# Kernel tuning notes

Measured on AMD Instinct MI355X. Metric: run time of the kernel, lower is better.

Reference implementation:

```python
import jax, jax.numpy as jnp
import numpy as np

B, H, W, DIM = 1, 256, 256, 192
HEADS = 6
K, DIL = 7, 2            # NAttention kernel / dilation
WS, DF = 8, 2            # stripe window size, anchor down factor
AWS = WS // DF           # anchor window size (4)
N1, N2 = WS * WS, AWS * AWS
L = H * W
CPB_HID = 512


def _nbr(size, k, d):
    # 1D neighborhood-attention neighbor indices with dilation (edge-clamped)
    i = np.arange(size); g = i % d; p = i // d
    gsize = size // d  # d divides size
    start = np.clip(p - k // 2, 0, gsize - k)
    nbr_p = start[:, None] + np.arange(k)[None, :]
    nbr = g[:, None] + d * nbr_p                    # absolute key index
    rb = nbr_p - p[:, None] + (k - 1)               # rpb index in [0, 2k-2]
    return nbr.astype(np.int32), rb.astype(np.int32)

NBR_H, RB_H = _nbr(H, K, DIL)
NBR_W, RB_W = _nbr(W, K, DIL)


def _na_attention(q, k, v, rpb):
    # q,k,v: (B, heads, H, W, hd); rpb: (heads, 2K-1, 2K-1)
    bias = rpb[:, RB_H, :]                          # (heads,H,K,2K-1)
    bias = jnp.take(bias, RB_W, axis=3)             # (heads,H,K,W,K)
    bias = jnp.transpose(bias, (0, 1, 3, 2, 4))     # (heads,H,W,K,K)
    logits = []
    for ki in range(K):
        kh = jnp.take(k, NBR_H[:, ki], axis=2)
        for kj in range(K):
            khw = jnp.take(kh, NBR_W[:, kj], axis=3)
            logits.append(jnp.einsum('bnhwc,bnhwc->bnhw', q, khw))
    a = jnp.stack(logits, axis=-1).reshape(*q.shape[:4], K, K) + bias[None]
    a = jax.nn.softmax(a.reshape(*q.shape[:4], K * K), axis=-1).reshape(*q.shape[:4], K, K)
    out = jnp.zeros_like(q)
    for ki in range(K):
        vh = jnp.take(v, NBR_H[:, ki], axis=2)
        for kj in range(K):
            vhw = jnp.take(vh, NBR_W[:, kj], axis=3)
            out = out + a[..., ki, kj, None] * vhw
    return out

na_attention = jax.checkpoint(_na_attention)


def window_partition(x, ws):
    b, h, w, c = x.shape
    x = x.reshape(b, h // ws, ws, w // ws, ws, c)
    return jnp.transpose(x, (0, 1, 3, 2, 4, 5)).reshape(-1, ws * ws, c)


def window_reverse(x, ws, h, w):
    c = x.shape[-1]
    b = x.shape[0] // ((h // ws) * (w // ws))
    x = x.reshape(b, h // ws, w // ws, ws, ws, c)
    return jnp.transpose(x, (0, 1, 3, 2, 4, 5)).reshape(b, h, w, c)


def _l2n(x):
    n = jnp.linalg.norm(x, axis=-1, keepdims=True)
    return x / jnp.maximum(n, 1e-12)


def _affine(attn, table, index, ls, w1, b1, w2):
    # attn: (Bw, heads, Na, Nb)
    attn = attn * jnp.exp(jnp.minimum(ls, float(np.log(100.0))))[None]
    bt = jax.nn.relu(table.reshape(-1, 2) @ w1 + b1) @ w2           # (T, heads)
    bias = bt[index.reshape(-1)].reshape(index.shape[0], index.shape[1], HEADS)
    bias = 16.0 * jax.nn.sigmoid(jnp.transpose(bias, (2, 0, 1)))    # (heads,Na,Nb)
    return attn + bias[None]


def _cos_attn(q, k, v, table, index, ls, w1, b1, w2):
    attn = jnp.einsum('bhnc,bhmc->bhnm', _l2n(q), _l2n(k))
    attn = jax.nn.softmax(_affine(attn, table, index, ls, w1, b1, w2), axis=-1)
    return attn @ v


def _forward(x, h_size, w_size, table, index_a2w, index_w2a, qkv_w, qkv_b,
             anchor_dw_w, anchor_dw_b, anchor_pw_w, anchor_pw_b,
             na_qkv_w, na_qkv_b, na_after_w, na_after_b, na_rpb,
             ls1, cpb1_w1, cpb1_b1, cpb1_w2, ls2, cpb2_w1, cpb2_b1, cpb2_w2,
             proj_w, proj_b):
    Bx, Lx, C = x.shape
    Hs, Ws_ = int(h_size), int(w_size)
    qkv = x @ qkv_w + qkv_b                     # (B,L,3C)
    half = C * 3 // 2
    qkv_window, qkv_stripe = qkv[..., :half], qkv[..., half:]
    # anchor projection: depthwise conv (k=DF+1, stride=DF) + pointwise
    xi = x.reshape(Bx, Hs, Ws_, C)
    a = jax.lax.conv_general_dilated(
        xi, anchor_dw_w, (DF, DF), ((1, 1), (1, 1)),
        dimension_numbers=('NHWC', 'HWIO', 'NHWC'), feature_group_count=C) + anchor_dw_b
    a = a @ anchor_pw_w + anchor_pw_b           # (B, H/DF, W/DF, C//2)
    # ---- neighborhood attention branch ----
    hd = C // HEADS
    xw = qkv_window.reshape(Bx, Hs, Ws_, half)
    q2 = (xw @ na_qkv_w + na_qkv_b).reshape(Bx, Hs, Ws_, 3, HEADS, hd)
    q2 = jnp.transpose(q2, (3, 0, 4, 1, 2, 5))  # (3,B,heads,H,W,hd)
    qn, kn, vn = q2[0] * hd ** -0.5, q2[1], q2[2]
    xna = na_attention(qn, kn, vn, na_rpb)
    xna = jnp.transpose(xna, (0, 2, 3, 1, 4)).reshape(Bx, Hs, Ws_, C)
    xna = (xna @ na_after_w + na_after_b).reshape(Bx, Lx, C // 2)
    # ---- anchor stripe attention branch ----
    qs = window_partition(qkv_stripe.reshape(Bx, Hs, Ws_, half), WS)  # (Bw,N1,1.5C)
    an = window_partition(a, AWS)                                     # (Bw,N2,C//2)
    Bw = qs.shape[0]
    hs = C // 2 // HEADS
    q3 = jnp.transpose(qs.reshape(Bw, N1, 3, HEADS, hs), (2, 0, 3, 1, 4))
    q_s, k_s, v_s = q3[0], q3[1], q3[2]
    an = jnp.transpose(an.reshape(Bw, N2, HEADS, hs), (0, 2, 1, 3))
    x1 = _cos_attn(an, k_s, v_s, table, index_a2w, ls1, cpb1_w1, cpb1_b1, cpb1_w2)
    x2 = _cos_attn(q_s, an, x1, table, index_w2a, ls2, cpb2_w1, cpb2_b1, cpb2_w2)
    x2 = jnp.transpose(x2, (0, 2, 1, 3)).reshape(Bw, N1, C // 2)
    xs = window_reverse(x2, WS, Hs, Ws_).reshape(Bx, Lx, C // 2)
    return jnp.concatenate([xna, xs], axis=-1) @ proj_w + proj_b


def setup_inputs() -> dict:
    key = jax.random.key(0)
    ks = jax.random.split(key, 16)
    f = lambda i, shp, s=0.02: jax.random.normal(ks[i], shp, dtype=jnp.float32) * s
    x = jax.random.normal(ks[0], (B, L, DIM), dtype=jnp.float32)
    # swin-v2 style normalized log-spaced relative coords table
    rc = np.arange(-(WS - 1), WS, dtype=np.float32) / (WS - 1)
    t = np.stack(np.meshgrid(rc, rc, indexing='ij'), axis=-1)[None]
    table = jnp.asarray(np.sign(t) * np.log2(1 + np.abs(t) * 8) / 3.0, dtype=jnp.float32)
    wc = np.arange(WS); ac = np.arange(AWS) * DF
    cw = np.stack(np.meshgrid(wc, wc, indexing='ij'), -1).reshape(-1, 2)
    ca = np.stack(np.meshgrid(ac, ac, indexing='ij'), -1).reshape(-1, 2)
    def _idx(c1, c2):
        d = c1[:, None, :] - c2[None, :, :]
        return jnp.asarray((d[..., 0] + WS - 1) * (2 * WS - 1) + (d[..., 1] + WS - 1), dtype=jnp.int32)
    return {
        'x': x, 'h_size': H, 'w_size': W, 'table': table,
        'index_a2w': _idx(ca, cw), 'index_w2a': _idx(cw, ca),
        'qkv_w': f(1, (DIM, 3 * DIM)), 'qkv_b': jnp.zeros((3 * DIM,), jnp.float32),
        'anchor_dw_w': f(2, (DF + 1, DF + 1, 1, DIM), 0.1),
        'anchor_dw_b': jnp.zeros((DIM,), jnp.float32),
        'anchor_pw_w': f(3, (DIM, DIM // 2)), 'anchor_pw_b': jnp.zeros((DIM // 2,), jnp.float32),
        'na_qkv_w': f(4, (3 * DIM // 2, 3 * DIM)), 'na_qkv_b': jnp.zeros((3 * DIM,), jnp.float32),
        'na_after_w': f(5, (DIM, DIM // 2)), 'na_after_b': jnp.zeros((DIM // 2,), jnp.float32),
        'na_rpb': f(6, (HEADS, 2 * K - 1, 2 * K - 1)),
        'ls1': jnp.log(10.0) * jnp.ones((HEADS, 1, 1), jnp.float32),
        'cpb1_w1': f(7, (2, CPB_HID), 0.1), 'cpb1_b1': jnp.zeros((CPB_HID,), jnp.float32),
        'cpb1_w2': f(8, (CPB_HID, HEADS), 0.1),
        'ls2': jnp.log(10.0) * jnp.ones((HEADS, 1, 1), jnp.float32),
        'cpb2_w1': f(9, (2, CPB_HID), 0.1), 'cpb2_b1': jnp.zeros((CPB_HID,), jnp.float32),
        'cpb2_w2': f(10, (CPB_HID, HEADS), 0.1),
        'proj_w': f(11, (DIM, DIM)), 'proj_b': jnp.zeros((DIM,), jnp.float32),
    }


def reference(x, h_size, w_size, table, index_a2w, index_w2a, qkv_w, qkv_b,
              anchor_dw_w, anchor_dw_b, anchor_pw_w, anchor_pw_b,
              na_qkv_w, na_qkv_b, na_after_w, na_after_b, na_rpb,
              ls1, cpb1_w1, cpb1_b1, cpb1_w2, ls2, cpb2_w1, cpb2_b1, cpb2_w2,
              proj_w, proj_b):
    return _forward(x, h_size, w_size, table, index_a2w, index_w2a, qkv_w, qkv_b,
                    anchor_dw_w, anchor_dw_b, anchor_pw_w, anchor_pw_b,
                    na_qkv_w, na_qkv_b, na_after_w, na_after_b, na_rpb,
                    ls1, cpb1_w1, cpb1_b1, cpb1_w2, ls2, cpb2_w1, cpb2_b1, cpb2_w2,
                    proj_w, proj_b)
```

## Files before the change

kernel.cpp:

```cpp
#include <hip/hip_runtime.h>
#include <math.h>


typedef unsigned short bf16_t;
typedef __attribute__((ext_vector_type(8))) short short8;
typedef __attribute__((ext_vector_type(4))) float f32x4;

__device__ inline float bf2f(bf16_t v) { return __uint_as_float((unsigned)v << 16); }
__device__ inline bf16_t f2bf(float f) {
    unsigned u = __float_as_uint(f);
    unsigned r = (u + 0x7fffu + ((u >> 16) & 1u)) >> 16;
    return (bf16_t)r;
}
__device__ inline float cvt(float v) { return v; }
__device__ inline float cvt(bf16_t v) { return bf2f(v); }
__device__ inline void sto(float* p, float v) { *p = v; }
__device__ inline void sto(bf16_t* p, float v) { *p = f2bf(v); }

__device__ inline void ld_bf8(const bf16_t* p, float* d) {
    uint4 r = *(const uint4*)p;
    d[0] = __uint_as_float(r.x << 16); d[1] = __uint_as_float(r.x & 0xffff0000u);
    d[2] = __uint_as_float(r.y << 16); d[3] = __uint_as_float(r.y & 0xffff0000u);
    d[4] = __uint_as_float(r.z << 16); d[5] = __uint_as_float(r.z & 0xffff0000u);
    d[6] = __uint_as_float(r.w << 16); d[7] = __uint_as_float(r.w & 0xffff0000u);
}
__device__ inline unsigned pk2(float a, float b) {
    return (unsigned)f2bf(a) | ((unsigned)f2bf(b) << 16);
}

template <int KD, int NA, typename TO>
__global__ __launch_bounds__(256) void mfma_gemm_k(
    const bf16_t* __restrict__ A, const bf16_t* __restrict__ Bt,
    const float* __restrict__ bias, TO* __restrict__ C,
    int lda, int ldb, int ldc)
{
    const int t = threadIdx.x;
    const int lane = t & 63, wave = t >> 6;
    const int wr = wave >> 1, wc = wave & 1;
    const int m0 = blockIdx.y * 128 + wr * 64;
    const int n0 = blockIdx.x * 96 + wc * 48;
    const int lm = lane & 15;
    const int q  = lane >> 4;

    f32x4 acc[4][3] = {};
    const bf16_t* ap = A + (size_t)(m0 + lm) * lda + q * 8;
    const bf16_t* bp = Bt + (size_t)(n0 + lm) * ldb + q * 8;

#pragma unroll
    for (int k0 = 0; k0 < KD; k0 += 32) {
        short8 af[4], bf[3];
#pragma unroll
        for (int mi = 0; mi < 4; mi++)
            af[mi] = *(const short8*)(ap + (size_t)(mi * 16) * lda + k0);
#pragma unroll
        for (int ni = 0; ni < 3; ni++)
            bf[ni] = *(const short8*)(bp + (size_t)(ni * 16) * ldb + k0);
#pragma unroll
        for (int mi = 0; mi < 4; mi++)
#pragma unroll
            for (int ni = 0; ni < 3; ni++)
                acc[mi][ni] = __builtin_amdgcn_mfma_f32_16x16x32_bf16(
                    af[mi], bf[ni], acc[mi][ni], 0, 0, 0);
    }

#pragma unroll
    for (int mi = 0; mi < 4; mi++) {
#pragma unroll
        for (int ni = 0; ni < 3; ni++) {
            int col = n0 + ni * 16 + lm;
            float bv = bias[col];
            if (NA) {
                int which = col / 192;
                int hh = (col % 192) / 32;
                int d  = col % 32;
                size_t pbase = ((size_t)which * 6 + hh) * ((size_t)65536 * 32) + d;
#pragma unroll
                for (int r = 0; r < 4; r++) {
                    int row = m0 + mi * 16 + q * 4 + r;
                    int ii = row >> 8, jj = row & 255;
                    int par = ((ii & 1) << 1) | (jj & 1);
                    int pix = par * 16384 + (ii >> 1) * 128 + (jj >> 1);
                    sto(&C[pbase + (size_t)pix * 32], acc[mi][ni][r] + bv);
                }
            } else {
#pragma unroll
                for (int r = 0; r < 4; r++) {
                    int row = m0 + mi * 16 + q * 4 + r;
                    sto(&C[(size_t)row * ldc + col], acc[mi][ni][r] + bv);
                }
            }
        }
    }
}

__global__ __launch_bounds__(256) void cvt_bf16_k(
    const float* __restrict__ src, bf16_t* __restrict__ dst, int n8)
{
    int tid = blockIdx.x * 256 + threadIdx.x;
    if (tid >= n8) return;
    float4 a = ((const float4*)src)[tid * 2];
    float4 b = ((const float4*)src)[tid * 2 + 1];
    uint4 o;
    o.x = pk2(a.x, a.y); o.y = pk2(a.z, a.w);
    o.z = pk2(b.x, b.y); o.w = pk2(b.z, b.w);
    ((uint4*)dst)[tid] = o;
}

__global__ __launch_bounds__(256) void tcvt_k(
    const float* __restrict__ W, bf16_t* __restrict__ Wt,
    int Kd, int N, int ld, int coloff)
{
    int tid = blockIdx.x * 256 + threadIdx.x;
    if (tid >= Kd * N) return;
    int k = tid % Kd, n = tid / Kd;
    Wt[tid] = f2bf(W[(size_t)k * ld + coloff + n]);
}

__global__ __launch_bounds__(256) void tpose_qkvw_k(
    const float* __restrict__ W, float* __restrict__ WT)
{
    int tid = blockIdx.x * 256 + threadIdx.x;
    if (tid >= 288 * 192) return;
    int k = tid % 192, j = tid / 192;
    WT[tid] = W[(size_t)k * 576 + j];
}

__global__ __launch_bounds__(256) void fold_wna_t_k(
    const float* __restrict__ qkv_wT, const float* __restrict__ na_qkv_w,
    bf16_t* __restrict__ Wna_t)
{
    int tid = blockIdx.x * 256 + threadIdx.x;
    if (tid >= 576 * 192) return;
    int k = tid % 192, n = tid / 192;
    float acc = 0.f;
    for (int j = 0; j < 288; j++)
        acc += qkv_wT[j * 192 + k] * na_qkv_w[j * 576 + n];
    Wna_t[tid] = f2bf(acc);
}

__global__ __launch_bounds__(256) void fold_bna_k(
    const float* __restrict__ qkv_b, const float* __restrict__ na_qkv_w,
    const float* __restrict__ na_qkv_b, float* __restrict__ bna)
{
    int j = blockIdx.x * 256 + threadIdx.x;
    if (j >= 576) return;
    float acc = na_qkv_b[j];
    for (int k = 0; k < 288; k++)
        acc += qkv_b[k] * na_qkv_w[k * 576 + j];
    bna[j] = acc;
}

__global__ __launch_bounds__(256) void cpb_k(
    const float* __restrict__ table, const float* __restrict__ w1,
    const float* __restrict__ b1, const float* __restrict__ w2,
    float* __restrict__ bt)
{
    int tid = blockIdx.x * 256 + threadIdx.x;
    if (tid >= 225 * 6) return;
    int h = tid % 6, t = tid / 6;
    float t0 = table[t * 2], t1 = table[t * 2 + 1];
    float acc = 0.f;
    for (int m = 0; m < 512; m++) {
        float hv = t0 * w1[m] + t1 * w1[512 + m] + b1[m];
        hv = fmaxf(hv, 0.f);
        acc += hv * w2[m * 6 + h];
    }
    bt[tid] = acc;
}

__global__ __launch_bounds__(256) void sigb_k(
    const float* __restrict__ bt, const int* __restrict__ idx,
    float* __restrict__ bp)
{
    int tid = blockIdx.x * 256 + threadIdx.x;
    if (tid >= 6144) return;
    int h = tid >> 10, p = tid & 1023;
    bp[tid] = 16.0f / (1.0f + __expf(-bt[idx[p] * 6 + h]));
}

#define BM 64
#define BN 64
#define BKK 16
template <typename TA, typename TO>
__global__ __launch_bounds__(256) void gemm_k(
    const TA* __restrict__ A, const float* __restrict__ B,
    const float* __restrict__ bias, TO* __restrict__ C,
    int M, int N, int Kd, int lda, int ldb, int ldc)
{
    __shared__ float As[BKK][BM + 1];
    __shared__ float Bs[BKK][BN + 1];
    const int t  = threadIdx.x;
    const int tx = t & 15, ty = t >> 4;
    const int m0 = blockIdx.y * BM, n0 = blockIdx.x * BN;
    float acc[4][4] = {};

    for (int k0 = 0; k0 < Kd; k0 += BKK) {
#pragma unroll
        for (int i = 0; i < 4; i++) {
            int m = (t >> 4) + i * 16;
            int k = t & 15;
            int gm = m0 + m, gk = k0 + k;
            As[k][m] = (gm < M && gk < Kd) ? cvt(A[(size_t)gm * lda + gk]) : 0.f;
        }
#pragma unroll
        for (int i = 0; i < 4; i++) {
            int k = (t >> 6) + i * 4;
            int n = t & 63;
            int gk = k0 + k, gn = n0 + n;
            Bs[k][n] = (gk < Kd && gn < N) ? B[(size_t)gk * ldb + gn] : 0.f;
        }
        __syncthreads();
#pragma unroll
        for (int k = 0; k < BKK; k++) {
            float a[4], b[4];
#pragma unroll
            for (int i = 0; i < 4; i++) a[i] = As[k][ty * 4 + i];
#pragma unroll
            for (int j = 0; j < 4; j++) b[j] = Bs[k][tx * 4 + j];
#pragma unroll
            for (int i = 0; i < 4; i++)
#pragma unroll
                for (int j = 0; j < 4; j++) acc[i][j] += a[i] * b[j];
        }
        __syncthreads();
    }
#pragma unroll
    for (int i = 0; i < 4; i++) {
        int gm = m0 + ty * 4 + i;
        if (gm >= M) continue;
#pragma unroll
        for (int j = 0; j < 4; j++) {
            int gn = n0 + tx * 4 + j;
            if (gn >= N) continue;
            sto(&C[(size_t)gm * ldc + gn], acc[i][j] + bias[gn]);
        }
    }
}

__global__ __launch_bounds__(256) void dwconv_k(
    const float* __restrict__ x, const float* __restrict__ w,
    const float* __restrict__ b, float* __restrict__ adw)
{
    int tid = blockIdx.x * 256 + threadIdx.x;
    if (tid >= 16384 * 48) return;
    int c4 = tid % 48;
    int p = tid / 48;
    int ow = p & 127, oh = p >> 7;
    int c = c4 * 4;
    float4 s = *(const float4*)(b + c);
#pragma unroll
    for (int kh = 0; kh < 3; kh++) {
        int ih = oh * 2 - 1 + kh;
        if (ih < 0 || ih >= 256) continue;
#pragma unroll
        for (int kw = 0; kw < 3; kw++) {
            int iw = ow * 2 - 1 + kw;
            if (iw < 0 || iw >= 256) continue;
            float4 xv = *(const float4*)(x + (size_t)(ih * 256 + iw) * 192 + c);
            float4 wv = *(const float4*)(w + (kh * 3 + kw) * 192 + c);
            s.x += xv.x * wv.x; s.y += xv.y * wv.y;
            s.z += xv.z * wv.z; s.w += xv.w * wv.w;
        }
    }
    *(float4*)(adw + (size_t)p * 192 + c) = s;
}

__global__ __launch_bounds__(256) void na_attn_k(
    const bf16_t* __restrict__ nap, const float* __restrict__ rpb,
    bf16_t* __restrict__ outp)
{
    __shared__ float rpb_s[176];
    __shared__ __align__(16) unsigned P_s[4][16][20];

    const int t = threadIdx.x;
    const int wv = t >> 6, lane = t & 63;
    const int lm = lane & 15, lq = lane >> 4;
    const int z = blockIdx.z;
    const int h = z >> 2, par = z & 3;

    if (t < 169) rpb_s[t] = rpb[h * 169 + t];
    __syncthreads();

    const int pi  = blockIdx.y;
    const int pj0 = blockIdx.x * 64 + wv * 16;
    const int si  = min(max(pi - 3, 0), 121);
    const int rbh0 = si - pi + 6;
    const int c0  = min(max(pj0 - 3, 0), 121) & ~7;

    const size_t plane = (size_t)65536 * 32;
    const size_t poff  = (size_t)(par * 16384) * 32;
    const bf16_t* qpl = nap + (size_t)h * plane + poff;
    const bf16_t* kpl = nap + (size_t)(6 + h) * plane + poff;
    const bf16_t* vpl = nap + (size_t)(12 + h) * plane + poff;

    const short8 qf = *(const short8*)(qpl + ((size_t)(pi * 128 + pj0 + lm)) * 32 + lq * 8);

    int offc[4][2]; bool vm[4][2];
#pragma unroll
    for (int r = 0; r < 4; r++) {
        int q = lq * 4 + r, pj = pj0 + q;
        int sj = min(max(pj - 3, 0), 121);
#pragma unroll
        for (int t2 = 0; t2 < 2; t2++) {
            int c = c0 + 2 * lm + t2;
            vm[r][t2] = (c >= sj) && (c <= sj + 6);
            offc[r][t2] = min(max(c - pj + 6, 0), 12);
        }
    }
    const int kc0 = min(c0 + 2 * lm,     127) * 64;
    const int kc1 = min(c0 + 2 * lm + 1, 127) * 64;
    int vcoff[8];
#pragma unroll
    for (int i = 0; i < 8; i++) vcoff[i] = min(c0 + lq * 8 + i, 127) * 64;

    const float scale = 0.17677669529663687f;
    f32x4 o0 = {}, o1 = {};
    float sums[4] = {0.f, 0.f, 0.f, 0.f};
    const f32x4 zz = {};

#pragma unroll 2
    for (int rr = 0; rr < 7; rr++) {
        const size_t rb2 = (size_t)((si + rr) * 128) * 64;
        const char* krow = (const char*)kpl + rb2;
        const char* vrow = (const char*)vpl + rb2;

        short8 kf0 = *(const short8*)(krow + kc0 + lq * 16);
        short8 kf1 = *(const short8*)(krow + kc1 + lq * 16);
        f32x4 s0 = __builtin_amdgcn_mfma_f32_16x16x32_bf16(qf, kf0, zz, 0, 0, 0);
        f32x4 s1 = __builtin_amdgcn_mfma_f32_16x16x32_bf16(qf, kf1, zz, 0, 0, 0);

        const float* br = rpb_s + (rbh0 + rr) * 13;
        float e0[4], e1[4];
#pragma unroll
        for (int r = 0; r < 4; r++) {
            float a0 = __expf(fmaf(s0[r], scale, br[offc[r][0]]));
            float a1 = __expf(fmaf(s1[r], scale, br[offc[r][1]]));
            a0 = vm[r][0] ? a0 : 0.f;
            a1 = vm[r][1] ? a1 : 0.f;
            e0[r] = a0; e1[r] = a1;
            sums[r] += a0 + a1;
        }
#pragma unroll
        for (int r = 0; r < 4; r++) {
            unsigned pr;
            asm("v_cvt_pk_bf16_f32 %0, %1, %2" : "=v"(pr) : "v"(e0[r]), "v"(e1[r]));
            P_s[wv][lq * 4 + r][lm] = pr;
        }
        const short8 pf = *(const short8*)((const bf16_t*)P_s[wv][lm] + lq * 8);

        short8 vf0, vf1;
        const char* v0b = vrow + lm * 2;
        const char* v1b = vrow + 32 + lm * 2;
#pragma unroll
        for (int i = 0; i < 8; i++) {
            ((bf16_t*)&vf0)[i] = *(const bf16_t*)(v0b + vcoff[i]);
            ((bf16_t*)&vf1)[i] = *(const bf16_t*)(v1b + vcoff[i]);
        }
        o0 = __builtin_amdgcn_mfma_f32_16x16x32_bf16(pf, vf0, o0, 0, 0, 0);
        o1 = __builtin_amdgcn_mfma_f32_16x16x32_bf16(pf, vf1, o1, 0, 0, 0);
    }

#pragma unroll
    for (int r = 0; r < 4; r++) {
        float s = sums[r];
        s += __shfl_xor(s, 1, 64);
        s += __shfl_xor(s, 2, 64);
        s += __shfl_xor(s, 4, 64);
        s += __shfl_xor(s, 8, 64);
        sums[r] = 1.0f / s;
    }

    const int gi = par >> 1, gj = par & 1;
    const int i0 = pi * 2 + gi;
    bf16_t* ob = outp + ((size_t)i0 * 256 + gj) * 192 + h * 32 + lm;
#pragma unroll
    for (int r = 0; r < 4; r++) {
        int q = lq * 4 + r;
        size_t px = (size_t)(pj0 + q) * 2 * 192;
        ob[px]      = f2bf(o0[r] * sums[r]);
        ob[px + 16] = f2bf(o1[r] * sums[r]);
    }
}

__global__ __launch_bounds__(256) void attn1_k(
    const float* __restrict__ apw,
    const bf16_t* __restrict__ qkvs,
    const float* __restrict__ b1p,
    const float* __restrict__ ls1,
    float* __restrict__ x1)
{
    int tid = blockIdx.x * 256 + threadIdx.x;
    int s  = tid & 7;
    int n2 = (tid >> 3) & 15;
    int h  = (tid >> 7) % 6;
    int w  = tid / 768;
    int wi = w >> 5, wj = w & 31;
    float scale = __expf(fminf(ls1[h], 4.605170185988091f));

    int ay = wi * 4 + (n2 >> 2), ax = wj * 4 + (n2 & 3);
    const float* ap = apw + (size_t)(ay * 128 + ax) * 96 + h * 16;
    float qv[16]; float nrm = 0.f;
#pragma unroll
    for (int d = 0; d < 16; d += 4) {
        float4 v = *(const float4*)(ap + d);
        qv[d] = v.x; qv[d + 1] = v.y; qv[d + 2] = v.z; qv[d + 3] = v.w;
        nrm += v.x * v.x + v.y * v.y + v.z * v.z + v.w * v.w;
    }
    float innorm = 1.0f / fmaxf(sqrtf(nrm), 1e-12f);
#pragma unroll
    for (int d = 0; d < 16; d++) qv[d] *= innorm;

    const float* bp = b1p + h * 1024 + n2 * 64 + s * 8;
    int ky = wi * 8 + s;
    const bf16_t* kbase = qkvs + (size_t)(ky * 256 + wj * 8) * 288 + 96 + h * 16;

    float sum = 0.f;
    float acc[16] = {};
#pragma unroll
    for (int j = 0; j < 8; j++) {
        const bf16_t* kp = kbase + j * 288;
        float kv[16];
        ld_bf8(kp, kv); ld_bf8(kp + 8, kv + 8);
        float dot = 0.f, kn = 0.f;
#pragma unroll
        for (int d = 0; d < 16; d++) { dot += qv[d] * kv[d]; kn += kv[d] * kv[d]; }
        dot *= 1.0f / fmaxf(sqrtf(kn), 1e-12f);
        float e = __expf(fmaf(dot, scale, bp[j]));
        sum += e;
        const bf16_t* vp = kp + 96;
        float vv[16];
        ld_bf8(vp, vv); ld_bf8(vp + 8, vv + 8);
#pragma unroll
        for (int d = 0; d < 16; d++) acc[d] += e * vv[d];
    }
#pragma unroll
    for (int msk = 1; msk < 8; msk <<= 1) {
        sum += __shfl_xor(sum, msk, 64);
#pragma unroll
        for (int d = 0; d < 16; d++) acc[d] += __shfl_xor(acc[d], msk, 64);
    }
    if (s == 0) {
        float inv = 1.0f / sum;
        float* xp = x1 + ((size_t)w * 6 + h) * 256 + n2 * 16;
#pragma unroll
        for (int d = 0; d < 16; d += 4)
            *(float4*)(xp + d) = make_float4(acc[d] * inv, acc[d + 1] * inv,
                                             acc[d + 2] * inv, acc[d + 3] * inv);
    }
}

__global__ __launch_bounds__(256) void attn2_k(
    const float* __restrict__ apw,
    const bf16_t* __restrict__ qkvs,
    const float* __restrict__ b2p,
    const float* __restrict__ ls2,
    const float* __restrict__ x1,
    bf16_t* __restrict__ cat)
{
    int tid = blockIdx.x * 256 + threadIdx.x;
    if (tid >= 1024 * 6 * 64) return;
    int n1 = tid & 63;
    int h = (tid >> 6) % 6;
    int w = tid / 384;
    int wi = w >> 5, wj = w & 31;
    float scale = __expf(fminf(ls2[h], 4.605170185988091f));

    int qy = wi * 8 + (n1 >> 3), qx = wj * 8 + (n1 & 7);
    const bf16_t* qp = qkvs + (size_t)(qy * 256 + qx) * 288 + h * 16;
    float qv[16];
    ld_bf8(qp, qv); ld_bf8(qp + 8, qv + 8);
    float nrm = 0.f;
#pragma unroll
    for (int d = 0; d < 16; d++) nrm += qv[d] * qv[d];
    float innorm = 1.0f / fmaxf(sqrtf(nrm), 1e-12f);
#pragma unroll
    for (int d = 0; d < 16; d++) qv[d] *= innorm;

    const float* bp = b2p + h * 1024 + n1 * 16;
    float sum = 0.f;
    float acc[16] = {};
#pragma unroll
    for (int m = 0; m < 16; m++) {
        int ay = wi * 4 + (m >> 2), ax = wj * 4 + (m & 3);
        const float* ap = apw + (size_t)(ay * 128 + ax) * 96 + h * 16;
        float dot = 0.f, kn = 0.f;
#pragma unroll
        for (int d = 0; d < 16; d += 4) {
            float4 v = *(const float4*)(ap + d);
            dot += qv[d] * v.x + qv[d + 1] * v.y + qv[d + 2] * v.z + qv[d + 3] * v.w;
            kn += v.x * v.x + v.y * v.y + v.z * v.z + v.w * v.w;
        }
        dot *= 1.0f / fmaxf(sqrtf(kn), 1e-12f);
        float e = __expf(fmaf(dot, scale, bp[m]));
        sum += e;
        const float* vp = x1 + ((size_t)w * 6 + h) * 256 + m * 16;
#pragma unroll
        for (int d = 0; d < 16; d += 4) {
            float4 v = *(const float4*)(vp + d);
            acc[d] += e * v.x; acc[d + 1] += e * v.y;
            acc[d + 2] += e * v.z; acc[d + 3] += e * v.w;
        }
    }
    float inv = 1.0f / sum;
#pragma unroll
    for (int d = 0; d < 16; d++) acc[d] *= inv;
    bf16_t* op = cat + (size_t)(qy * 256 + qx) * 192 + 96 + h * 16;
    uint4 o0, o1;
    o0.x = pk2(acc[0], acc[1]);   o0.y = pk2(acc[2], acc[3]);
    o0.z = pk2(acc[4], acc[5]);   o0.w = pk2(acc[6], acc[7]);
    o1.x = pk2(acc[8], acc[9]);   o1.y = pk2(acc[10], acc[11]);
    o1.z = pk2(acc[12], acc[13]); o1.w = pk2(acc[14], acc[15]);
    *(uint4*)(op) = o0;
    *(uint4*)(op + 8) = o1;
}

extern "C" void kernel_launch(void* const* d_in, const int* in_sizes, int n_in,
                              void* d_out, int out_size, void* d_ws, size_t ws_size,
                              hipStream_t stream) {
    const float* x          = (const float*)d_in[0];
    const float* table      = (const float*)d_in[3];
    const int*   idx_a2w    = (const int*)d_in[4];
    const int*   idx_w2a    = (const int*)d_in[5];
    const float* qkv_w      = (const float*)d_in[6];
    const float* qkv_b      = (const float*)d_in[7];
    const float* adw_w      = (const float*)d_in[8];
    const float* adw_b      = (const float*)d_in[9];
    const float* apw_w      = (const float*)d_in[10];
    const float* apw_b      = (const float*)d_in[11];
    const float* na_qkv_w   = (const float*)d_in[12];
    const float* na_qkv_b   = (const float*)d_in[13];
    const float* na_after_w = (const float*)d_in[14];
    const float* na_after_b = (const float*)d_in[15];
    const float* na_rpb     = (const float*)d_in[16];
    const float* ls1        = (const float*)d_in[17];
    const float* cpb1_w1    = (const float*)d_in[18];
    const float* cpb1_b1    = (const float*)d_in[19];
    const float* cpb1_w2    = (const float*)d_in[20];
    const float* ls2        = (const float*)d_in[21];
    const float* cpb2_w1    = (const float*)d_in[22];
    const float* cpb2_b1    = (const float*)d_in[23];
    const float* cpb2_w2    = (const float*)d_in[24];
    const float* proj_w     = (const float*)d_in[25];
    const float* proj_b     = (const float*)d_in[26];
    float* out = (float*)d_out;
    (void)in_sizes; (void)n_in; (void)out_size; (void)ws_size;

    char* base = (char*)d_ws;
    size_t off = 0;
    auto alloc = [&](size_t bytes) {
        off = (off + 255) & ~(size_t)255;
        void* p = base + off; off += bytes; return p;
    };
    float*  bna    = (float*)alloc(576 * 4);
    float*  bt1    = (float*)alloc(225 * 6 * 4);
    float*  bt2    = (float*)alloc(225 * 6 * 4);
    float*  b1p    = (float*)alloc(6144 * 4);
    float*  b2p    = (float*)alloc(6144 * 4);
    float*  qkv_wT = (float*)alloc(288 * 192 * 4);
    bf16_t* Wna_t  = (bf16_t*)alloc(576 * 192 * 2);
    bf16_t* Ws_t   = (bf16_t*)alloc(288 * 192 * 2);
    bf16_t* Waft_t = (bf16_t*)alloc(96 * 192 * 2);
    bf16_t* Wproj_t= (bf16_t*)alloc(192 * 192 * 2);
    bf16_t* qkvs   = (bf16_t*)alloc((size_t)65536 * 288 * 2);
    char*   naR    = (char*)alloc((size_t)65536 * 576 * 2);
    char*   R      = (char*)alloc((size_t)65536 * 192 * 2);
    float*  apw    = (float*)alloc((size_t)16384 * 96 * 4);
    bf16_t* naqkv   = (bf16_t*)naR;
    float*  x1      = (float*)naR;
    bf16_t* cat     = (bf16_t*)(naR + (8 << 20));
    bf16_t* xb      = (bf16_t*)R;
    float*  adw     = (float*)R;
    bf16_t* xna_pre = (bf16_t*)R;

    tpose_qkvw_k<<<216, 256, 0, stream>>>(qkv_w, qkv_wT);
    fold_wna_t_k<<<432, 256, 0, stream>>>(qkv_wT, na_qkv_w, Wna_t);
    fold_bna_k<<<3, 256, 0, stream>>>(qkv_b, na_qkv_w, na_qkv_b, bna);
    cpb_k<<<6, 256, 0, stream>>>(table, cpb1_w1, cpb1_b1, cpb1_w2, bt1);
    cpb_k<<<6, 256, 0, stream>>>(table, cpb2_w1, cpb2_b1, cpb2_w2, bt2);
    sigb_k<<<24, 256, 0, stream>>>(bt1, idx_a2w, b1p);
    sigb_k<<<24, 256, 0, stream>>>(bt2, idx_w2a, b2p);
    tcvt_k<<<216, 256, 0, stream>>>(qkv_w, Ws_t, 192, 288, 576, 288);
    tcvt_k<<<72, 256, 0, stream>>>(na_after_w, Waft_t, 192, 96, 96, 0);
    tcvt_k<<<144, 256, 0, stream>>>(proj_w, Wproj_t, 192, 192, 192, 0);
    cvt_bf16_k<<<6144, 256, 0, stream>>>(x, xb, 65536 * 192 / 8);

    mfma_gemm_k<192, 0, bf16_t><<<dim3(3, 512), 256, 0, stream>>>(
        xb, Ws_t, qkv_b + 288, qkvs, 192, 192, 288);

    mfma_gemm_k<192, 1, bf16_t><<<dim3(6, 512), 256, 0, stream>>>(
        xb, Wna_t, bna, naqkv, 192, 192, 576);

    dwconv_k<<<3072, 256, 0, stream>>>(x, adw_w, adw_b, adw);
    gemm_k<float, float><<<dim3(2, 256), 256, 0, stream>>>(
        adw, apw_w, apw_b, apw, 16384, 96, 192, 192, 96, 96);

    na_attn_k<<<dim3(2, 128, 24), 256, 0, stream>>>(naqkv, na_rpb, xna_pre);

    mfma_gemm_k<192, 0, bf16_t><<<dim3(1, 512), 256, 0, stream>>>(
        xna_pre, Waft_t, na_after_b, cat, 192, 192, 192);

    attn1_k<<<3072, 256, 0, stream>>>(apw, qkvs, b1p, ls1, x1);
    attn2_k<<<1536, 256, 0, stream>>>(apw, qkvs, b2p, ls2, x1, cat);

    mfma_gemm_k<192, 0, float><<<dim3(2, 512), 256, 0, stream>>>(
        cat, Wproj_t, proj_b, out, 192, 192, 192);
}
```

Measured before the change: 666.5 us.

## Rewrite anchor-to-window attention with bf16 MFMA and transposed bias table

Replaces the scalar per-thread attn1 kernel with a wave-per-window kernel that computes QK logits and the PV product using 16x16x32 bf16 MFMA instructions. Probabilities are staged through shared memory and the bias is preloaded into LDS. A new bias kernel writes a transposed bias layout to match the MFMA output layout. This cuts scalar FMA and shuffle reductions, but rounds normalized q/k and the probabilities to bf16, which lowers precision.

```diff
diff --git a/kernel.cpp b/kernel.cpp
--- a/kernel.cpp
+++ b/kernel.cpp
@@ -178,6 +178,17 @@
     bp[tid] = 16.0f / (1.0f + __expf(-bt[idx[p] * 6 + h]));
 }
 
+__global__ __launch_bounds__(256) void sigb1T_k(
+    const float* __restrict__ bt, const int* __restrict__ idx,
+    float* __restrict__ bp)
+{
+    int tid = blockIdx.x * 256 + threadIdx.x;
+    if (tid >= 6144) return;
+    int h = tid >> 10, p = tid & 1023;
+    int m = p >> 4, n2 = p & 15;
+    bp[tid] = 16.0f / (1.0f + __expf(-bt[idx[n2 * 64 + m] * 6 + h]));
+}
+
 #define BM 64
 #define BN 64
 #define BKK 16
@@ -385,67 +396,113 @@
 __global__ __launch_bounds__(256) void attn1_k(
     const float* __restrict__ apw,
     const bf16_t* __restrict__ qkvs,
-    const float* __restrict__ b1p,
+    const float* __restrict__ b1pT,
     const float* __restrict__ ls1,
     float* __restrict__ x1)
 {
-    int tid = blockIdx.x * 256 + threadIdx.x;
-    int s  = tid & 7;
-    int n2 = (tid >> 3) & 15;
-    int h  = (tid >> 7) % 6;
-    int w  = tid / 768;
-    int wi = w >> 5, wj = w & 31;
-    float scale = __expf(fminf(ls1[h], 4.605170185988091f));
-
-    int ay = wi * 4 + (n2 >> 2), ax = wj * 4 + (n2 & 3);
-    const float* ap = apw + (size_t)(ay * 128 + ax) * 96 + h * 16;
-    float qv[16]; float nrm = 0.f;
-#pragma unroll
-    for (int d = 0; d < 16; d += 4) {
-        float4 v = *(const float4*)(ap + d);
-        qv[d] = v.x; qv[d + 1] = v.y; qv[d + 2] = v.z; qv[d + 3] = v.w;
-        nrm += v.x * v.x + v.y * v.y + v.z * v.z + v.w * v.w;
-    }
-    float innorm = 1.0f / fmaxf(sqrtf(nrm), 1e-12f);
-#pragma unroll
-    for (int d = 0; d < 16; d++) qv[d] *= innorm;
-
-    const float* bp = b1p + h * 1024 + n2 * 64 + s * 8;
-    int ky = wi * 8 + s;
-    const bf16_t* kbase = qkvs + (size_t)(ky * 256 + wj * 8) * 288 + 96 + h * 16;
-
+    __shared__ float bT_s[1024];
+    __shared__ __align__(16) unsigned P_s[4][16][36];
+
+    const int t = threadIdx.x;
+    const int wv = t >> 6, lane = t & 63;
+    const int lm = lane & 15, lq = lane >> 4;
+    const int h = blockIdx.y;
+    const int w = blockIdx.x * 4 + wv;
+    const int wi = w >> 5, wj = w & 31;
+
+#pragma unroll
+    for (int i = 0; i < 4; i++) bT_s[i * 256 + t] = b1pT[h * 1024 + i * 256 + t];
+    __syncthreads();
+
+    const float scale = __expf(fminf(ls1[h], 4.605170185988091f));
+
+    short8 af = {};
+    float an2 = 0.f;
+    {
+        int ay = wi * 4 + (lm >> 2), ax = wj * 4 + (lm & 3);
+        const float* ap = apw + (size_t)(ay * 128 + ax) * 96 + h * 16;
+        if (lq < 2) {
+            float4 v0 = *(const float4*)(ap + lq * 8);
+            float4 v1 = *(const float4*)(ap + lq * 8 + 4);
+            float vs[8] = {v0.x, v0.y, v0.z, v0.w, v1.x, v1.y, v1.z, v1.w};
+            unsigned* au = (unsigned*)&af;
+#pragma unroll
+            for (int j2 = 0; j2 < 4; j2++) {
+                unsigned u = pk2(vs[2 * j2], vs[2 * j2 + 1]);
+                au[j2] = u;
+                float lo = __uint_as_float(u << 16);
+                float hi = __uint_as_float(u & 0xffff0000u);
+                an2 += lo * lo + hi * hi;
+            }
+        }
+    }
+    an2 += __shfl_xor(an2, 16, 64);
+    an2 += __shfl_xor(an2, 32, 64);
+    const float sa = scale / fmaxf(sqrtf(an2), 1e-12f);
+
+    const f32x4 zz = {};
+    f32x4 o = {};
     float sum = 0.f;
-    float acc[16] = {};
-#pragma unroll
-    for (int j = 0; j < 8; j++) {
-        const bf16_t* kp = kbase + j * 288;
-        float kv[16];
-        ld_bf8(kp, kv); ld_bf8(kp + 8, kv + 8);
-        float dot = 0.f, kn = 0.f;
-#pragma unroll
-        for (int d = 0; d < 16; d++) { dot += qv[d] * kv[d]; kn += kv[d] * kv[d]; }
-        dot *= 1.0f / fmaxf(sqrtf(kn), 1e-12f);
-        float e = __expf(fmaf(dot, scale, bp[j]));
-        sum += e;
-        const bf16_t* vp = kp + 96;
-        float vv[16];
-        ld_bf8(vp, vv); ld_bf8(vp + 8, vv + 8);
-#pragma unroll
-        for (int d = 0; d < 16; d++) acc[d] += e * vv[d];
-    }
-#pragma unroll
-    for (int msk = 1; msk < 8; msk <<= 1) {
-        sum += __shfl_xor(sum, msk, 64);
-#pragma unroll
-        for (int d = 0; d < 16; d++) acc[d] += __shfl_xor(acc[d], msk, 64);
-    }
-    if (s == 0) {
-        float inv = 1.0f / sum;
-        float* xp = x1 + ((size_t)w * 6 + h) * 256 + n2 * 16;
-#pragma unroll
-        for (int d = 0; d < 16; d += 4)
-            *(float4*)(xp + d) = make_float4(acc[d] * inv, acc[d + 1] * inv,
-                                             acc[d + 2] * inv, acc[d + 3] * inv);
+
+#pragma unroll
+    for (int g = 0; g < 2; g++) {
+#pragma unroll
+        for (int tt = 0; tt < 2; tt++) {
+            const int tile = g * 2 + tt;
+            int py = wi * 8 + tile * 2 + (lm >> 3);
+            int px = wj * 8 + (lm & 7);
+            const bf16_t* kp = qkvs + (size_t)(py * 256 + px) * 288 + 96 + h * 16;
+            short8 kf = {};
+            float kn2 = 0.f;
+            float klo[4], khi[4];
+            if (lq < 2) {
+                uint4 kr = *(const uint4*)(kp + lq * 8);
+                unsigned ku[4] = {kr.x, kr.y, kr.z, kr.w};
+#pragma unroll
+                for (int j2 = 0; j2 < 4; j2++) {
+                    klo[j2] = __uint_as_float(ku[j2] << 16);
+                    khi[j2] = __uint_as_float(ku[j2] & 0xffff0000u);
+                    kn2 += klo[j2] * klo[j2] + khi[j2] * khi[j2];
+                }
+            }
+            kn2 += __shfl_xor(kn2, 16, 64);
+            kn2 += __shfl_xor(kn2, 32, 64);
+            float rk = 1.0f / fmaxf(sqrtf(kn2), 1e-12f);
+            if (lq < 2) {
+                unsigned* kuo = (unsigned*)&kf;
+#pragma unroll
+                for (int j2 = 0; j2 < 4; j2++)
+                    kuo[j2] = pk2(klo[j2] * rk, khi[j2] * rk);
+            }
+            f32x4 s = __builtin_amdgcn_mfma_f32_16x16x32_bf16(kf, af, zz, 0, 0, 0);
+            float e[4];
+#pragma unroll
+            for (int r = 0; r < 4; r++) {
+                e[r] = __expf(fmaf(s[r], sa,
+                              bT_s[((tile * 16 + lq * 4 + r) << 4) + lm]));
+                sum += e[r];
+            }
+            P_s[wv][lm][tile * 8 + lq * 2]     = pk2(e[0], e[1]);
+            P_s[wv][lm][tile * 8 + lq * 2 + 1] = pk2(e[2], e[3]);
+        }
+        const short8 pf = *(const short8*)&P_s[wv][lm][g * 16 + lq * 4];
+        short8 vf;
+        int pyv = wi * 8 + g * 4 + lq;
+        const bf16_t* vrow = qkvs + (size_t)(pyv * 256 + wj * 8) * 288 + 192 + h * 16 + lm;
+#pragma unroll
+        for (int i = 0; i < 8; i++)
+            ((bf16_t*)&vf)[i] = vrow[(size_t)i * 288];
+        o = __builtin_amdgcn_mfma_f32_16x16x32_bf16(pf, vf, o, 0, 0, 0);
+    }
+
+    sum += __shfl_xor(sum, 16, 64);
+    sum += __shfl_xor(sum, 32, 64);
+    const float inv = 1.0f / sum;
+    float* xp = x1 + ((size_t)w * 6 + h) * 256;
+#pragma unroll
+    for (int r = 0; r < 4; r++) {
+        float iv = __shfl(inv, lq * 4 + r, 64);
+        xp[(lq * 4 + r) * 16 + lm] = o[r] * iv;
     }
 }
 
@@ -554,7 +611,7 @@
     float*  bna    = (float*)alloc(576 * 4);
     float*  bt1    = (float*)alloc(225 * 6 * 4);
     float*  bt2    = (float*)alloc(225 * 6 * 4);
-    float*  b1p    = (float*)alloc(6144 * 4);
+    float*  b1pT   = (float*)alloc(6144 * 4);
     float*  b2p    = (float*)alloc(6144 * 4);
     float*  qkv_wT = (float*)alloc(288 * 192 * 4);
     bf16_t* Wna_t  = (bf16_t*)alloc(576 * 192 * 2);
@@ -577,7 +634,7 @@
     fold_bna_k<<<3, 256, 0, stream>>>(qkv_b, na_qkv_w, na_qkv_b, bna);
     cpb_k<<<6, 256, 0, stream>>>(table, cpb1_w1, cpb1_b1, cpb1_w2, bt1);
     cpb_k<<<6, 256, 0, stream>>>(table, cpb2_w1, cpb2_b1, cpb2_w2, bt2);
-    sigb_k<<<24, 256, 0, stream>>>(bt1, idx_a2w, b1p);
+    sigb1T_k<<<24, 256, 0, stream>>>(bt1, idx_a2w, b1pT);
     sigb_k<<<24, 256, 0, stream>>>(bt2, idx_w2a, b2p);
     tcvt_k<<<216, 256, 0, stream>>>(qkv_w, Ws_t, 192, 288, 576, 288);
     tcvt_k<<<72, 256, 0, stream>>>(na_after_w, Waft_t, 192, 96, 96, 0);
@@ -599,7 +656,7 @@
     mfma_gemm_k<192, 0, bf16_t><<<dim3(1, 512), 256, 0, stream>>>(
         xna_pre, Waft_t, na_after_b, cat, 192, 192, 192);
 
-    attn1_k<<<3072, 256, 0, stream>>>(apw, qkvs, b1p, ls1, x1);
+    attn1_k<<<dim3(256, 6), 256, 0, stream>>>(apw, qkvs, b1pT, ls1, x1);
     attn2_k<<<1536, 256, 0, stream>>>(apw, qkvs, b2p, ls2, x1, cat);
 
     mfma_gemm_k<192, 0, float><<<dim3(2, 512), 256, 0, stream>>>(
```

Result: faster. 600.8 us (-9.9%).
